# Kernel optimization log

Hardware: AMD Instinct MI355X
Metric: run time of the kernel (lower is better)

## Reference

```python
import jax, jax.numpy as jnp
import numpy as np

DIM = 256
HEADS = 4
HEAD_DIM = DIM // HEADS
WIN_DIC = {512: 16, 256: 16, 128: 8, 64: 8, 32: 4, 16: 4}


def window_partition(x, w):
    # x: [B, C, H, W] -> [B*nH*nW, w*w, C]
    B, C, H, W = x.shape
    x = x.reshape(B, C, H // w, w, W // w, w)
    x = jnp.transpose(x, (0, 2, 4, 3, 5, 1))
    return x.reshape(-1, w * w, C)


def window_reverse(windows, w, H, W, C):
    # windows: [B*nH*nW, w*w, C] -> [B, C, H, W]
    B = windows.shape[0] // ((H // w) * (W // w))
    x = windows.reshape(B, H // w, W // w, w, w, C)
    x = jnp.transpose(x, (0, 5, 1, 3, 2, 4))
    return x.reshape(B, C, H, W)


def setup_inputs() -> dict:
    key = jax.random.key(0)
    ks = jax.random.split(key, 10)
    B, C, H, W = 8, DIM, 128, 128
    feat_a = jax.random.normal(ks[0], (B, C, H, W), dtype=jnp.float32)
    feat_b = jax.random.normal(ks[1], (B, C, H, W), dtype=jnp.float32)
    s = 1.0 / np.sqrt(DIM)
    Wq = jax.random.normal(ks[2], (DIM, DIM), dtype=jnp.float32) * s
    bq = jnp.zeros((DIM,), dtype=jnp.float32)
    Wk = jax.random.normal(ks[3], (DIM, DIM), dtype=jnp.float32) * s
    bk = jnp.zeros((DIM,), dtype=jnp.float32)
    Wv = jax.random.normal(ks[4], (DIM, DIM), dtype=jnp.float32) * s
    bv = jnp.zeros((DIM,), dtype=jnp.float32)
    Wo = jax.random.normal(ks[5], (DIM, DIM), dtype=jnp.float32) * s
    bo = jnp.zeros((DIM,), dtype=jnp.float32)
    return {"feat_a": feat_a, "feat_b": feat_b, "Wq": Wq, "bq": bq,
            "Wk": Wk, "bk": bk, "Wv": Wv, "bv": bv, "Wo": Wo, "bo": bo}


def reference(feat_a, feat_b, Wq, bq, Wk, bk, Wv, bv, Wo, bo):
    B, C, H, W = feat_a.shape
    w = WIN_DIC[H]
    pad_h = (w - H % w) % w
    pad_w = (w - W % w) % w
    if pad_h or pad_w:
        feat_a = jnp.pad(feat_a, ((0, 0), (0, 0), (0, pad_h), (0, pad_w)), mode="reflect")
        feat_b = jnp.pad(feat_b, ((0, 0), (0, 0), (0, pad_h), (0, pad_w)), mode="reflect")
    Hp, Wp = feat_a.shape[2], feat_a.shape[3]

    qw = window_partition(feat_a, w)   # [B_, N, C]
    kw = window_partition(feat_b, w)
    # Linear (torch nn.Linear: x @ W.T + b)
    q = qw @ Wq.T + bq
    k = kw @ Wk.T + bk
    v = kw @ Wv.T + bv

    B_, N, _ = q.shape
    q = q.reshape(B_, N, HEADS, HEAD_DIM).transpose(0, 2, 1, 3)  # [B_, h, N, d]
    k = k.reshape(B_, N, HEADS, HEAD_DIM).transpose(0, 2, 1, 3)
    v = v.reshape(B_, N, HEADS, HEAD_DIM).transpose(0, 2, 1, 3)

    scale = HEAD_DIM ** -0.5
    attn = jnp.einsum("bhnd,bhmd->bhnm", q, k) * scale
    attn = jax.nn.softmax(attn, axis=-1)  # dropout is identity in eval mode
    out = jnp.einsum("bhnm,bhmd->bhnd", attn, v)
    out = out.transpose(0, 2, 1, 3).reshape(B_, N, C)
    out = out @ Wo.T + bo
    out = window_reverse(out, w, Hp, Wp, C)
    out = out[:, :, :H, :W]
    return (out, attn)
```

## Files before the change

### kernel.cpp

```cpp
#include <hip/hip_runtime.h>
#include <hip/hip_bf16.h>


typedef __bf16 bf16x8 __attribute__((ext_vector_type(8)));
typedef float f32x4 __attribute__((ext_vector_type(4)));
typedef unsigned short u16;
typedef unsigned short u16x8 __attribute__((ext_vector_type(8)));

#define MFMA16(A, B, C) __builtin_amdgcn_mfma_f32_16x16x32_bf16((A), (B), (C), 0, 0, 0)

__device__ __forceinline__ int swzA(int t, int byteInRow) {
    return (t << 9) + (byteInRow ^ ((((t & 7) ^ (t >> 3)) & 7) << 4));
}
__device__ __forceinline__ int swzB(int r, int byteInRow) {
    return (r << 7) + (byteInRow ^ ((((r & 7) ^ (r >> 3)) & 7) << 4));
}

__global__ __launch_bounds__(256) void pack_weights(
    const float* __restrict__ Wq, const float* __restrict__ Wk,
    const float* __restrict__ Wv, const float* __restrict__ Wo,
    __bf16* __restrict__ pk)
{
    int gid = blockIdx.x * 256 + threadIdx.x;
    int m = gid >> 13;
    int f = gid & 8191;
    const float* W = (m == 0) ? Wq : (m == 1) ? Wk : (m == 2) ? Wv : Wo;
    int q  = f >> 11;
    int kk = (f >> 8) & 7;
    int t16 = (f >> 6) & 3;
    int l  = f & 63;
    int row = (q << 6) + (t16 << 4) + (l & 15);
    int col = (kk << 5) + ((l >> 4) << 3);
    const float* s = W + row * 256 + col;
    f32x4 a = *(const f32x4*)s;
    f32x4 b = *(const f32x4*)(s + 4);
    bf16x8 r;
    r[0] = (__bf16)a[0]; r[1] = (__bf16)a[1]; r[2] = (__bf16)a[2]; r[3] = (__bf16)a[3];
    r[4] = (__bf16)b[0]; r[5] = (__bf16)b[1]; r[6] = (__bf16)b[2]; r[7] = (__bf16)b[3];
    *(bf16x8*)(pk + (size_t)gid * 8) = r;
}

__device__ __forceinline__ bf16x8 loadWP(const __bf16* __restrict__ pk,
                                         int q, int kk, int t16, int l) {
    return *(const bf16x8*)(pk + ((((q << 3) + kk) << 2) + t16) * 512 + (l << 3));
}

__global__ __launch_bounds__(512) void wca_fused(
    const float* __restrict__ fa, const float* __restrict__ fb,
    const __bf16* __restrict__ WPq, const float* __restrict__ bq,
    const __bf16* __restrict__ WPk, const float* __restrict__ bk,
    const __bf16* __restrict__ WPv, const float* __restrict__ bv,
    const __bf16* __restrict__ WPo, const float* __restrict__ bo,
    float* __restrict__ outg, float* __restrict__ attng)
{
    __shared__ __attribute__((aligned(16))) char S[131072];
    char* const XA = S;
    char* const XB = S + 32768;
    char* const QQ = S + 65536;
    char* const KK = S + 98304;

    const int tid  = threadIdx.x;
    const int l    = tid & 63;
    const int wid  = tid >> 6;
    const int lrow = l & 15;
    const int kg   = l >> 4;
    const int q    = wid & 3;
    const int th   = wid >> 2;

    const int wgid = blockIdx.x;
    const int win  = ((wgid & 7) << 8) | (wgid >> 3);
    const int b    = win >> 8;
    const int wy   = (win >> 4) & 15;
    const int wx   = win & 15;
    const int ybase = wy << 3, xbase = wx << 3;

    {
        #pragma unroll
        for (int f = 0; f < 2; ++f) {
            const float* src = f ? fb : fa;
            char* dst = f ? XB : XA;
            #pragma unroll
            for (int it = 0; it < 4; ++it) {
                int idx = (it << 9) + tid;
                int c  = idx >> 3;
                int ty = idx & 7;
                const float* gp = src + ((((size_t)b * 256 + c) * 128 + ybase + ty) * 128 + xbase);
                f32x4 v0 = *(const f32x4*)gp;
                f32x4 v1 = *(const f32x4*)(gp + 4);
                #pragma unroll
                for (int tx = 0; tx < 4; ++tx) {
                    int t0 = (ty << 3) + tx;
                    int t1 = (ty << 3) + 4 + tx;
                    *(__bf16*)(dst + swzA(t0, c << 1)) = (__bf16)v0[tx];
                    *(__bf16*)(dst + swzA(t1, c << 1)) = (__bf16)v1[tx];
                }
            }
        }
    }
    __syncthreads();

    {
        #pragma unroll
        for (int pp = 0; pp < 2; ++pp) {
            const __bf16* WP  = pp ? WPk : WPq;
            const float* bias = pp ? bk : bq;
            const char* Xs  = pp ? XB : XA;
            char* dstR      = pp ? KK : QQ;
            f32x4 acc[2][4] = {};
            #pragma unroll
            for (int kk = 0; kk < 8; ++kk) {
                int c0 = (kk << 5) + (kg << 3);
                bf16x8 a0 = *(const bf16x8*)(Xs + swzA((th << 5) + lrow,      c0 << 1));
                bf16x8 a1 = *(const bf16x8*)(Xs + swzA((th << 5) + 16 + lrow, c0 << 1));
                #pragma unroll
                for (int nt = 0; nt < 4; ++nt) {
                    bf16x8 bb = loadWP(WP, q, kk, nt, l);
                    acc[0][nt] = MFMA16(a0, bb, acc[0][nt]);
                    acc[1][nt] = MFMA16(a1, bb, acc[1][nt]);
                }
            }
            #pragma unroll
            for (int mt = 0; mt < 2; ++mt) {
                #pragma unroll
                for (int nt = 0; nt < 4; ++nt) {
                    int co = (q << 6) + (nt << 4) + lrow;
                    float bi = bias[co];
                    #pragma unroll
                    for (int r = 0; r < 4; ++r) {
                        int t = (th << 5) + (mt << 4) + (kg << 2) + r;
                        *(__bf16*)(dstR + swzA(t, co << 1)) = (__bf16)(acc[mt][nt][r] + bi);
                    }
                }
            }
        }
    }
    __syncthreads();

    {
        const int h = q;
        f32x4 s[2][4] = {};
        #pragma unroll
        for (int kk = 0; kk < 2; ++kk) {
            int c0 = (h << 6) + (kk << 5) + (kg << 3);
            bf16x8 a0 = *(const bf16x8*)(QQ + swzA((th << 5) + lrow,      c0 << 1));
            bf16x8 a1 = *(const bf16x8*)(QQ + swzA((th << 5) + 16 + lrow, c0 << 1));
            #pragma unroll
            for (int nt = 0; nt < 4; ++nt) {
                bf16x8 kb = *(const bf16x8*)(KK + swzA((nt << 4) + lrow, c0 << 1));
                s[0][nt] = MFMA16(a0, kb, s[0][nt]);
                s[1][nt] = MFMA16(a1, kb, s[1][nt]);
            }
        }
        const float CS = 0.125f * 1.44269504f;
        #pragma unroll
        for (int mt = 0; mt < 2; ++mt) {
            #pragma unroll
            for (int r = 0; r < 4; ++r) {
                float mx = fmaxf(fmaxf(s[mt][0][r], s[mt][1][r]),
                                 fmaxf(s[mt][2][r], s[mt][3][r]));
                mx = fmaxf(mx, __shfl_xor(mx, 1));
                mx = fmaxf(mx, __shfl_xor(mx, 2));
                mx = fmaxf(mx, __shfl_xor(mx, 4));
                mx = fmaxf(mx, __shfl_xor(mx, 8));
                float p0 = exp2f((s[mt][0][r] - mx) * CS);
                float p1 = exp2f((s[mt][1][r] - mx) * CS);
                float p2 = exp2f((s[mt][2][r] - mx) * CS);
                float p3 = exp2f((s[mt][3][r] - mx) * CS);
                float sm = (p0 + p1) + (p2 + p3);
                sm += __shfl_xor(sm, 1);
                sm += __shfl_xor(sm, 2);
                sm += __shfl_xor(sm, 4);
                sm += __shfl_xor(sm, 8);
                float inv = 1.0f / sm;
                int i = (th << 5) + (mt << 4) + (kg << 2) + r;
                char* pb = XA + (h << 13);
                *(__bf16*)(pb + swzB(i, ((0 << 4) + lrow) << 1)) = (__bf16)(p0 * inv);
                *(__bf16*)(pb + swzB(i, ((1 << 4) + lrow) << 1)) = (__bf16)(p1 * inv);
                *(__bf16*)(pb + swzB(i, ((2 << 4) + lrow) << 1)) = (__bf16)(p2 * inv);
                *(__bf16*)(pb + swzB(i, ((3 << 4) + lrow) << 1)) = (__bf16)(p3 * inv);
            }
        }
    }
    __syncthreads();

    {
        f32x4 acc[4][2] = {};
        #pragma unroll
        for (int kk = 0; kk < 8; ++kk) {
            int c0 = (kk << 5) + (kg << 3);
            bf16x8 bx0 = *(const bf16x8*)(XB + swzA((th << 5) + lrow,      c0 << 1));
            bf16x8 bx1 = *(const bf16x8*)(XB + swzA((th << 5) + 16 + lrow, c0 << 1));
            #pragma unroll
            for (int mt = 0; mt < 4; ++mt) {
                bf16x8 aw = loadWP(WPv, q, kk, mt, l);
                acc[mt][0] = MFMA16(aw, bx0, acc[mt][0]);
                acc[mt][1] = MFMA16(aw, bx1, acc[mt][1]);
            }
        }
        #pragma unroll
        for (int mt = 0; mt < 4; ++mt) {
            #pragma unroll
            for (int r = 0; r < 4; ++r) {
                int vc = (q << 6) + (mt << 4) + (kg << 2) + r;
                float bi = bv[vc];
                #pragma unroll
                for (int nt = 0; nt < 2; ++nt) {
                    int t = (th << 5) + (nt << 4) + lrow;
                    *(__bf16*)(QQ + swzB(vc, t << 1)) = (__bf16)(acc[mt][nt][r] + bi);
                }
            }
        }
        #pragma unroll
        for (int it = 0; it < 4; ++it) {
            int idx = (it << 9) + tid;
            int h2 = idx >> 9;
            int i2 = (idx >> 3) & 63;
            int jb = (idx & 7) << 3;
            u16x8 v = *(const u16x8*)(XA + (h2 << 13) + swzB(i2, jb << 1));
            float* dp = attng + ((((size_t)(win << 2) + h2) << 6) + i2) * 64 + jb;
            f32x4 o0, o1;
            #pragma unroll
            for (int e = 0; e < 4; ++e) {
                union { unsigned u; float f; } c0; c0.u = (unsigned)v[e] << 16;
                union { unsigned u; float f; } c1; c1.u = (unsigned)v[4 + e] << 16;
                o0[e] = c0.f; o1[e] = c1.f;
            }
            *(f32x4*)dp = o0;
            *(f32x4*)(dp + 4) = o1;
        }
    }
    __syncthreads();

    {
        const int h = q;
        f32x4 o[2][4] = {};
        #pragma unroll
        for (int kk = 0; kk < 2; ++kk) {
            int j0 = (kk << 5) + (kg << 3);
            bf16x8 a0 = *(const bf16x8*)(XA + (h << 13) + swzB((th << 5) + lrow,      j0 << 1));
            bf16x8 a1 = *(const bf16x8*)(XA + (h << 13) + swzB((th << 5) + 16 + lrow, j0 << 1));
            #pragma unroll
            for (int dt = 0; dt < 4; ++dt) {
                bf16x8 vb = *(const bf16x8*)(QQ + swzB((h << 6) + (dt << 4) + lrow, j0 << 1));
                o[0][dt] = MFMA16(a0, vb, o[0][dt]);
                o[1][dt] = MFMA16(a1, vb, o[1][dt]);
            }
        }
        #pragma unroll
        for (int mt = 0; mt < 2; ++mt) {
            #pragma unroll
            for (int dt = 0; dt < 4; ++dt) {
                #pragma unroll
                for (int r = 0; r < 4; ++r) {
                    int t = (th << 5) + (mt << 4) + (kg << 2) + r;
                    int c = (h << 6) + (dt << 4) + lrow;
                    *(__bf16*)(KK + swzA(t, c << 1)) = (__bf16)o[mt][dt][r];
                }
            }
        }
    }
    __syncthreads();

    {
        f32x4 acc[4][2] = {};
        #pragma unroll
        for (int kk = 0; kk < 8; ++kk) {
            int k0 = (kk << 5) + (kg << 3);
            bf16x8 b0 = *(const bf16x8*)(KK + swzA((th << 5) + lrow,      k0 << 1));
            bf16x8 b1 = *(const bf16x8*)(KK + swzA((th << 5) + 16 + lrow, k0 << 1));
            #pragma unroll
            for (int mt = 0; mt < 4; ++mt) {
                bf16x8 aw = loadWP(WPo, q, kk, mt, l);
                acc[mt][0] = MFMA16(aw, b0, acc[mt][0]);
                acc[mt][1] = MFMA16(aw, b1, acc[mt][1]);
            }
        }
        #pragma unroll
        for (int mt = 0; mt < 4; ++mt) {
            #pragma unroll
            for (int r = 0; r < 4; ++r) {
                int c = (q << 6) + (mt << 4) + (kg << 2) + r;
                float bi = bo[c];
                #pragma unroll
                for (int nt = 0; nt < 2; ++nt) {
                    int t = (th << 5) + (nt << 4) + lrow;
                    int y = ybase + (t >> 3);
                    int x = xbase + (t & 7);
                    size_t off = (((size_t)b * 256 + c) * 128 + y) * 128 + x;
                    outg[off] = acc[mt][nt][r] + bi;
                }
            }
        }
    }
}

extern "C" void kernel_launch(void* const* d_in, const int* in_sizes, int n_in,
                              void* d_out, int out_size, void* d_ws, size_t ws_size,
                              hipStream_t stream) {
    (void)in_sizes; (void)n_in; (void)ws_size; (void)out_size;
    const float* fa = (const float*)d_in[0];
    const float* fb = (const float*)d_in[1];
    const float* Wq = (const float*)d_in[2];
    const float* bq = (const float*)d_in[3];
    const float* Wk = (const float*)d_in[4];
    const float* bk = (const float*)d_in[5];
    const float* Wv = (const float*)d_in[6];
    const float* bv = (const float*)d_in[7];
    const float* Wo = (const float*)d_in[8];
    const float* bo = (const float*)d_in[9];
    float* outg  = (float*)d_out;
    float* attng = outg + (size_t)8 * 256 * 128 * 128;

    __bf16* pk = (__bf16*)d_ws;
    const __bf16* WPq = pk;
    const __bf16* WPk = pk + 65536;
    const __bf16* WPv = pk + 131072;
    const __bf16* WPo = pk + 196608;

    pack_weights<<<dim3(128), dim3(256), 0, stream>>>(Wq, Wk, Wv, Wo, pk);
    wca_fused<<<dim3(2048), dim3(512), 0, stream>>>(
        fa, fb, WPq, bq, WPk, bk, WPv, bv, WPo, bo, outg, attng);
}
```

Measured before the change: 310.4 us.

## Halve LDS footprint by holding K, V, P in registers and reusing two regions

Shared memory per block shrinks from 128 KB to 64 KB. The K, V and softmax P results are held in packed bf16 registers across barriers, and two LDS regions are reused for each stage, so more workgroups can be resident per CU. The launch bounds now request 4 waves per SIMD. Attention probabilities are written to global as fp32 directly from registers instead of through an LDS round trip, and the values are no longer rounded to bf16. The cost is more barriers, higher register pressure and less coalesced scattered global stores for attn.

```diff
diff --git a/kernel.cpp b/kernel.cpp
--- a/kernel.cpp
+++ b/kernel.cpp
@@ -5,7 +5,6 @@
 typedef __bf16 bf16x8 __attribute__((ext_vector_type(8)));
 typedef float f32x4 __attribute__((ext_vector_type(4)));
 typedef unsigned short u16;
-typedef unsigned short u16x8 __attribute__((ext_vector_type(8)));
 
 #define MFMA16(A, B, C) __builtin_amdgcn_mfma_f32_16x16x32_bf16((A), (B), (C), 0, 0, 0)
 
@@ -14,6 +13,10 @@
 }
 __device__ __forceinline__ int swzB(int r, int byteInRow) {
     return (r << 7) + (byteInRow ^ ((((r & 7) ^ (r >> 3)) & 7) << 4));
+}
+__device__ __forceinline__ u16 bfbits(float x) {
+    __bf16 h = (__bf16)x;
+    return *(u16*)&h;
 }
 
 __global__ __launch_bounds__(256) void pack_weights(
@@ -45,7 +48,7 @@
     return *(const bf16x8*)(pk + ((((q << 3) + kk) << 2) + t16) * 512 + (l << 3));
 }
 
-__global__ __launch_bounds__(512) void wca_fused(
+__global__ __launch_bounds__(512, 4) void wca_fused(
     const float* __restrict__ fa, const float* __restrict__ fb,
     const __bf16* __restrict__ WPq, const float* __restrict__ bq,
     const __bf16* __restrict__ WPk, const float* __restrict__ bk,
@@ -53,11 +56,9 @@
     const __bf16* __restrict__ WPo, const float* __restrict__ bo,
     float* __restrict__ outg, float* __restrict__ attng)
 {
-    __shared__ __attribute__((aligned(16))) char S[131072];
-    char* const XA = S;
-    char* const XB = S + 32768;
-    char* const QQ = S + 65536;
-    char* const KK = S + 98304;
+    __shared__ __attribute__((aligned(16))) char S[65536];
+    char* const R1 = S;
+    char* const R2 = S + 32768;
 
     const int tid  = threadIdx.x;
     const int l    = tid & 63;
@@ -78,7 +79,7 @@
         #pragma unroll
         for (int f = 0; f < 2; ++f) {
             const float* src = f ? fb : fa;
-            char* dst = f ? XB : XA;
+            char* dst = f ? R2 : R1;
             #pragma unroll
             for (int it = 0; it < 4; ++it) {
                 int idx = (it << 9) + tid;
@@ -89,64 +90,133 @@
                 f32x4 v1 = *(const f32x4*)(gp + 4);
                 #pragma unroll
                 for (int tx = 0; tx < 4; ++tx) {
-                    int t0 = (ty << 3) + tx;
-                    int t1 = (ty << 3) + 4 + tx;
-                    *(__bf16*)(dst + swzA(t0, c << 1)) = (__bf16)v0[tx];
-                    *(__bf16*)(dst + swzA(t1, c << 1)) = (__bf16)v1[tx];
-                }
-            }
-        }
-    }
-    __syncthreads();
-
-    {
-        #pragma unroll
-        for (int pp = 0; pp < 2; ++pp) {
-            const __bf16* WP  = pp ? WPk : WPq;
-            const float* bias = pp ? bk : bq;
-            const char* Xs  = pp ? XB : XA;
-            char* dstR      = pp ? KK : QQ;
-            f32x4 acc[2][4] = {};
+                    *(__bf16*)(dst + swzA((ty << 3) + tx,     c << 1)) = (__bf16)v0[tx];
+                    *(__bf16*)(dst + swzA((ty << 3) + 4 + tx, c << 1)) = (__bf16)v1[tx];
+                }
+            }
+        }
+    }
+    __syncthreads();
+
+    f32x4 qacc[2][4] = {};
+    {
+        #pragma unroll
+        for (int kk = 0; kk < 8; ++kk) {
+            int c0 = (kk << 5) + (kg << 3);
+            bf16x8 a0 = *(const bf16x8*)(R1 + swzA((th << 5) + lrow,      c0 << 1));
+            bf16x8 a1 = *(const bf16x8*)(R1 + swzA((th << 5) + 16 + lrow, c0 << 1));
+            #pragma unroll
+            for (int nt = 0; nt < 4; ++nt) {
+                bf16x8 bb = loadWP(WPq, q, kk, nt, l);
+                qacc[0][nt] = MFMA16(a0, bb, qacc[0][nt]);
+                qacc[1][nt] = MFMA16(a1, bb, qacc[1][nt]);
+            }
+        }
+    }
+    __syncthreads();
+
+    unsigned kpk[16], vpk[16];
+    {
+        #pragma unroll
+        for (int mt = 0; mt < 2; ++mt) {
+            #pragma unroll
+            for (int nt = 0; nt < 4; ++nt) {
+                int co = (q << 6) + (nt << 4) + lrow;
+                float bi = bq[co];
+                #pragma unroll
+                for (int r = 0; r < 4; ++r) {
+                    int t = (th << 5) + (mt << 4) + (kg << 2) + r;
+                    *(__bf16*)(R1 + swzA(t, co << 1)) = (__bf16)(qacc[mt][nt][r] + bi);
+                }
+            }
+        }
+        {
+            f32x4 kacc[2][4] = {};
             #pragma unroll
             for (int kk = 0; kk < 8; ++kk) {
                 int c0 = (kk << 5) + (kg << 3);
-                bf16x8 a0 = *(const bf16x8*)(Xs + swzA((th << 5) + lrow,      c0 << 1));
-                bf16x8 a1 = *(const bf16x8*)(Xs + swzA((th << 5) + 16 + lrow, c0 << 1));
+                bf16x8 a0 = *(const bf16x8*)(R2 + swzA((th << 5) + lrow,      c0 << 1));
+                bf16x8 a1 = *(const bf16x8*)(R2 + swzA((th << 5) + 16 + lrow, c0 << 1));
                 #pragma unroll
                 for (int nt = 0; nt < 4; ++nt) {
-                    bf16x8 bb = loadWP(WP, q, kk, nt, l);
-                    acc[0][nt] = MFMA16(a0, bb, acc[0][nt]);
-                    acc[1][nt] = MFMA16(a1, bb, acc[1][nt]);
+                    bf16x8 bb = loadWP(WPk, q, kk, nt, l);
+                    kacc[0][nt] = MFMA16(a0, bb, kacc[0][nt]);
+                    kacc[1][nt] = MFMA16(a1, bb, kacc[1][nt]);
                 }
             }
             #pragma unroll
             for (int mt = 0; mt < 2; ++mt) {
                 #pragma unroll
                 for (int nt = 0; nt < 4; ++nt) {
-                    int co = (q << 6) + (nt << 4) + lrow;
-                    float bi = bias[co];
-                    #pragma unroll
-                    for (int r = 0; r < 4; ++r) {
-                        int t = (th << 5) + (mt << 4) + (kg << 2) + r;
-                        *(__bf16*)(dstR + swzA(t, co << 1)) = (__bf16)(acc[mt][nt][r] + bi);
-                    }
-                }
-            }
-        }
-    }
-    __syncthreads();
-
+                    float bi = bk[(q << 6) + (nt << 4) + lrow];
+                    kpk[(mt * 4 + nt) * 2 + 0] =
+                        (unsigned)bfbits(kacc[mt][nt][0] + bi) |
+                        ((unsigned)bfbits(kacc[mt][nt][1] + bi) << 16);
+                    kpk[(mt * 4 + nt) * 2 + 1] =
+                        (unsigned)bfbits(kacc[mt][nt][2] + bi) |
+                        ((unsigned)bfbits(kacc[mt][nt][3] + bi) << 16);
+                }
+            }
+        }
+        {
+            f32x4 vacc[4][2] = {};
+            #pragma unroll
+            for (int kk = 0; kk < 8; ++kk) {
+                int c0 = (kk << 5) + (kg << 3);
+                bf16x8 bx0 = *(const bf16x8*)(R2 + swzA((th << 5) + lrow,      c0 << 1));
+                bf16x8 bx1 = *(const bf16x8*)(R2 + swzA((th << 5) + 16 + lrow, c0 << 1));
+                #pragma unroll
+                for (int mt = 0; mt < 4; ++mt) {
+                    bf16x8 aw = loadWP(WPv, q, kk, mt, l);
+                    vacc[mt][0] = MFMA16(aw, bx0, vacc[mt][0]);
+                    vacc[mt][1] = MFMA16(aw, bx1, vacc[mt][1]);
+                }
+            }
+            #pragma unroll
+            for (int mt = 0; mt < 4; ++mt) {
+                #pragma unroll
+                for (int nt = 0; nt < 2; ++nt) {
+                    u16 w0 = bfbits(vacc[mt][nt][0] + bv[(q << 6) + (mt << 4) + (kg << 2) + 0]);
+                    u16 w1 = bfbits(vacc[mt][nt][1] + bv[(q << 6) + (mt << 4) + (kg << 2) + 1]);
+                    u16 w2 = bfbits(vacc[mt][nt][2] + bv[(q << 6) + (mt << 4) + (kg << 2) + 2]);
+                    u16 w3 = bfbits(vacc[mt][nt][3] + bv[(q << 6) + (mt << 4) + (kg << 2) + 3]);
+                    vpk[(mt * 2 + nt) * 2 + 0] = (unsigned)w0 | ((unsigned)w1 << 16);
+                    vpk[(mt * 2 + nt) * 2 + 1] = (unsigned)w2 | ((unsigned)w3 << 16);
+                }
+            }
+        }
+    }
+    __syncthreads();
+
+    {
+        #pragma unroll
+        for (int mt = 0; mt < 2; ++mt) {
+            #pragma unroll
+            for (int nt = 0; nt < 4; ++nt) {
+                int co = (q << 6) + (nt << 4) + lrow;
+                #pragma unroll
+                for (int r = 0; r < 4; ++r) {
+                    int t = (th << 5) + (mt << 4) + (kg << 2) + r;
+                    u16 val = (u16)(kpk[(mt * 4 + nt) * 2 + (r >> 1)] >> ((r & 1) * 16));
+                    *(u16*)(R2 + swzA(t, co << 1)) = val;
+                }
+            }
+        }
+    }
+    __syncthreads();
+
+    unsigned ppk[16];
     {
         const int h = q;
         f32x4 s[2][4] = {};
         #pragma unroll
         for (int kk = 0; kk < 2; ++kk) {
             int c0 = (h << 6) + (kk << 5) + (kg << 3);
-            bf16x8 a0 = *(const bf16x8*)(QQ + swzA((th << 5) + lrow,      c0 << 1));
-            bf16x8 a1 = *(const bf16x8*)(QQ + swzA((th << 5) + 16 + lrow, c0 << 1));
+            bf16x8 a0 = *(const bf16x8*)(R1 + swzA((th << 5) + lrow,      c0 << 1));
+            bf16x8 a1 = *(const bf16x8*)(R1 + swzA((th << 5) + 16 + lrow, c0 << 1));
             #pragma unroll
             for (int nt = 0; nt < 4; ++nt) {
-                bf16x8 kb = *(const bf16x8*)(KK + swzA((nt << 4) + lrow, c0 << 1));
+                bf16x8 kb = *(const bf16x8*)(R2 + swzA((nt << 4) + lrow, c0 << 1));
                 s[0][nt] = MFMA16(a0, kb, s[0][nt]);
                 s[1][nt] = MFMA16(a1, kb, s[1][nt]);
             }
@@ -172,29 +242,29 @@
                 sm += __shfl_xor(sm, 4);
                 sm += __shfl_xor(sm, 8);
                 float inv = 1.0f / sm;
+                p0 *= inv; p1 *= inv; p2 *= inv; p3 *= inv;
                 int i = (th << 5) + (mt << 4) + (kg << 2) + r;
-                char* pb = XA + (h << 13);
-                *(__bf16*)(pb + swzB(i, ((0 << 4) + lrow) << 1)) = (__bf16)(p0 * inv);
-                *(__bf16*)(pb + swzB(i, ((1 << 4) + lrow) << 1)) = (__bf16)(p1 * inv);
-                *(__bf16*)(pb + swzB(i, ((2 << 4) + lrow) << 1)) = (__bf16)(p2 * inv);
-                *(__bf16*)(pb + swzB(i, ((3 << 4) + lrow) << 1)) = (__bf16)(p3 * inv);
-            }
-        }
-    }
-    __syncthreads();
-
-    {
-        f32x4 acc[4][2] = {};
-        #pragma unroll
-        for (int kk = 0; kk < 8; ++kk) {
-            int c0 = (kk << 5) + (kg << 3);
-            bf16x8 bx0 = *(const bf16x8*)(XB + swzA((th << 5) + lrow,      c0 << 1));
-            bf16x8 bx1 = *(const bf16x8*)(XB + swzA((th << 5) + 16 + lrow, c0 << 1));
-            #pragma unroll
-            for (int mt = 0; mt < 4; ++mt) {
-                bf16x8 aw = loadWP(WPv, q, kk, mt, l);
-                acc[mt][0] = MFMA16(aw, bx0, acc[mt][0]);
-                acc[mt][1] = MFMA16(aw, bx1, acc[mt][1]);
+                float* ap = attng + (((size_t)(win << 2) + h) * 64 + i) * 64 + lrow;
+                ap[0] = p0; ap[16] = p1; ap[32] = p2; ap[48] = p3;
+                ppk[(mt * 4 + r) * 2 + 0] = (unsigned)bfbits(p0) | ((unsigned)bfbits(p1) << 16);
+                ppk[(mt * 4 + r) * 2 + 1] = (unsigned)bfbits(p2) | ((unsigned)bfbits(p3) << 16);
+            }
+        }
+    }
+    __syncthreads();
+
+    {
+        const int h = q;
+        #pragma unroll
+        for (int mt = 0; mt < 2; ++mt) {
+            #pragma unroll
+            for (int r = 0; r < 4; ++r) {
+                int i = (th << 5) + (mt << 4) + (kg << 2) + r;
+                #pragma unroll
+                for (int nt = 0; nt < 4; ++nt) {
+                    u16 val = (u16)(ppk[(mt * 4 + r) * 2 + (nt >> 1)] >> ((nt & 1) * 16));
+                    *(u16*)(R2 + (h << 13) + swzB(i, ((nt << 4) + lrow) << 1)) = val;
+                }
             }
         }
         #pragma unroll
@@ -202,50 +272,37 @@
             #pragma unroll
             for (int r = 0; r < 4; ++r) {
                 int vc = (q << 6) + (mt << 4) + (kg << 2) + r;
-                float bi = bv[vc];
                 #pragma unroll
                 for (int nt = 0; nt < 2; ++nt) {
                     int t = (th << 5) + (nt << 4) + lrow;
-                    *(__bf16*)(QQ + swzB(vc, t << 1)) = (__bf16)(acc[mt][nt][r] + bi);
-                }
-            }
-        }
-        #pragma unroll
-        for (int it = 0; it < 4; ++it) {
-            int idx = (it << 9) + tid;
-            int h2 = idx >> 9;
-            int i2 = (idx >> 3) & 63;
-            int jb = (idx & 7) << 3;
-            u16x8 v = *(const u16x8*)(XA + (h2 << 13) + swzB(i2, jb << 1));
-            float* dp = attng + ((((size_t)(win << 2) + h2) << 6) + i2) * 64 + jb;
-            f32x4 o0, o1;
-            #pragma unroll
-            for (int e = 0; e < 4; ++e) {
-                union { unsigned u; float f; } c0; c0.u = (unsigned)v[e] << 16;
-                union { unsigned u; float f; } c1; c1.u = (unsigned)v[4 + e] << 16;
-                o0[e] = c0.f; o1[e] = c1.f;
-            }
-            *(f32x4*)dp = o0;
-            *(f32x4*)(dp + 4) = o1;
-        }
-    }
-    __syncthreads();
-
+                    u16 val = (u16)(vpk[(mt * 2 + nt) * 2 + (r >> 1)] >> ((r & 1) * 16));
+                    *(u16*)(R1 + swzB(vc, t << 1)) = val;
+                }
+            }
+        }
+    }
+    __syncthreads();
+
+    f32x4 o[2][4] = {};
     {
         const int h = q;
-        f32x4 o[2][4] = {};
         #pragma unroll
         for (int kk = 0; kk < 2; ++kk) {
             int j0 = (kk << 5) + (kg << 3);
-            bf16x8 a0 = *(const bf16x8*)(XA + (h << 13) + swzB((th << 5) + lrow,      j0 << 1));
-            bf16x8 a1 = *(const bf16x8*)(XA + (h << 13) + swzB((th << 5) + 16 + lrow, j0 << 1));
+            bf16x8 a0 = *(const bf16x8*)(R2 + (h << 13) + swzB((th << 5) + lrow,      j0 << 1));
+            bf16x8 a1 = *(const bf16x8*)(R2 + (h << 13) + swzB((th << 5) + 16 + lrow, j0 << 1));
             #pragma unroll
             for (int dt = 0; dt < 4; ++dt) {
-                bf16x8 vb = *(const bf16x8*)(QQ + swzB((h << 6) + (dt << 4) + lrow, j0 << 1));
+                bf16x8 vb = *(const bf16x8*)(R1 + swzB((h << 6) + (dt << 4) + lrow, j0 << 1));
                 o[0][dt] = MFMA16(a0, vb, o[0][dt]);
                 o[1][dt] = MFMA16(a1, vb, o[1][dt]);
             }
         }
+    }
+    __syncthreads();
+
+    {
+        const int h = q;
         #pragma unroll
         for (int mt = 0; mt < 2; ++mt) {
             #pragma unroll
@@ -254,7 +311,7 @@
                 for (int r = 0; r < 4; ++r) {
                     int t = (th << 5) + (mt << 4) + (kg << 2) + r;
                     int c = (h << 6) + (dt << 4) + lrow;
-                    *(__bf16*)(KK + swzA(t, c << 1)) = (__bf16)o[mt][dt][r];
+                    *(__bf16*)(R1 + swzA(t, c << 1)) = (__bf16)o[mt][dt][r];
                 }
             }
         }
@@ -266,8 +323,8 @@
         #pragma unroll
         for (int kk = 0; kk < 8; ++kk) {
             int k0 = (kk << 5) + (kg << 3);
-            bf16x8 b0 = *(const bf16x8*)(KK + swzA((th << 5) + lrow,      k0 << 1));
-            bf16x8 b1 = *(const bf16x8*)(KK + swzA((th << 5) + 16 + lrow, k0 << 1));
+            bf16x8 b0 = *(const bf16x8*)(R1 + swzA((th << 5) + lrow,      k0 << 1));
+            bf16x8 b1 = *(const bf16x8*)(R1 + swzA((th << 5) + 16 + lrow, k0 << 1));
             #pragma unroll
             for (int mt = 0; mt < 4; ++mt) {
                 bf16x8 aw = loadWP(WPo, q, kk, mt, l);
```

After: 485.5 us. 56.4% more time.

## Reorder stages and shared buffers, request two workgroups per CU

Applied to the files above, without the earlier changes.

Adds a launch bound of two 512-thread workgroups per CU and reschedules the fused kernel. The V projection now runs right after Q/K, the attention probabilities go into the freed feat_b buffer, and the P·V product is merged into the same phase as the attention write-out, removing one barrier. The goal is fewer synchronisations and more resident waves. The 128 KB static shared allocation per workgroup may still prevent two workgroups from fitting on a CU, and the tighter register cap could cause spills.

```diff
diff --git a/kernel.cpp b/kernel.cpp
--- a/kernel.cpp
+++ b/kernel.cpp
@@ -45,7 +45,7 @@
     return *(const bf16x8*)(pk + ((((q << 3) + kk) << 2) + t16) * 512 + (l << 3));
 }
 
-__global__ __launch_bounds__(512) void wca_fused(
+__global__ __launch_bounds__(512, 2) void wca_fused(
     const float* __restrict__ fa, const float* __restrict__ fb,
     const __bf16* __restrict__ WPq, const float* __restrict__ bq,
     const __bf16* __restrict__ WPk, const float* __restrict__ bk,
@@ -54,10 +54,10 @@
     float* __restrict__ outg, float* __restrict__ attng)
 {
     __shared__ __attribute__((aligned(16))) char S[131072];
-    char* const XA = S;
-    char* const XB = S + 32768;
-    char* const QQ = S + 65536;
-    char* const KK = S + 98304;
+    char* const A = S;
+    char* const B = S + 32768;
+    char* const C = S + 65536;
+    char* const D = S + 98304;
 
     const int tid  = threadIdx.x;
     const int l    = tid & 63;
@@ -78,7 +78,7 @@
         #pragma unroll
         for (int f = 0; f < 2; ++f) {
             const float* src = f ? fb : fa;
-            char* dst = f ? XB : XA;
+            char* dst = f ? B : A;
             #pragma unroll
             for (int it = 0; it < 4; ++it) {
                 int idx = (it << 9) + tid;
@@ -89,47 +89,94 @@
                 f32x4 v1 = *(const f32x4*)(gp + 4);
                 #pragma unroll
                 for (int tx = 0; tx < 4; ++tx) {
-                    int t0 = (ty << 3) + tx;
-                    int t1 = (ty << 3) + 4 + tx;
-                    *(__bf16*)(dst + swzA(t0, c << 1)) = (__bf16)v0[tx];
-                    *(__bf16*)(dst + swzA(t1, c << 1)) = (__bf16)v1[tx];
-                }
-            }
-        }
-    }
-    __syncthreads();
-
-    {
-        #pragma unroll
-        for (int pp = 0; pp < 2; ++pp) {
-            const __bf16* WP  = pp ? WPk : WPq;
-            const float* bias = pp ? bk : bq;
-            const char* Xs  = pp ? XB : XA;
-            char* dstR      = pp ? KK : QQ;
-            f32x4 acc[2][4] = {};
-            #pragma unroll
-            for (int kk = 0; kk < 8; ++kk) {
-                int c0 = (kk << 5) + (kg << 3);
-                bf16x8 a0 = *(const bf16x8*)(Xs + swzA((th << 5) + lrow,      c0 << 1));
-                bf16x8 a1 = *(const bf16x8*)(Xs + swzA((th << 5) + 16 + lrow, c0 << 1));
-                #pragma unroll
-                for (int nt = 0; nt < 4; ++nt) {
-                    bf16x8 bb = loadWP(WP, q, kk, nt, l);
-                    acc[0][nt] = MFMA16(a0, bb, acc[0][nt]);
-                    acc[1][nt] = MFMA16(a1, bb, acc[1][nt]);
-                }
-            }
-            #pragma unroll
-            for (int mt = 0; mt < 2; ++mt) {
-                #pragma unroll
-                for (int nt = 0; nt < 4; ++nt) {
-                    int co = (q << 6) + (nt << 4) + lrow;
-                    float bi = bias[co];
-                    #pragma unroll
-                    for (int r = 0; r < 4; ++r) {
-                        int t = (th << 5) + (mt << 4) + (kg << 2) + r;
-                        *(__bf16*)(dstR + swzA(t, co << 1)) = (__bf16)(acc[mt][nt][r] + bi);
-                    }
+                    *(__bf16*)(dst + swzA((ty << 3) + tx,     c << 1)) = (__bf16)v0[tx];
+                    *(__bf16*)(dst + swzA((ty << 3) + 4 + tx, c << 1)) = (__bf16)v1[tx];
+                }
+            }
+        }
+    }
+    __syncthreads();
+
+    {
+        f32x4 qacc[2][4] = {};
+        #pragma unroll
+        for (int kk = 0; kk < 8; ++kk) {
+            int c0 = (kk << 5) + (kg << 3);
+            bf16x8 a0 = *(const bf16x8*)(A + swzA((th << 5) + lrow,      c0 << 1));
+            bf16x8 a1 = *(const bf16x8*)(A + swzA((th << 5) + 16 + lrow, c0 << 1));
+            #pragma unroll
+            for (int nt = 0; nt < 4; ++nt) {
+                bf16x8 bb = loadWP(WPq, q, kk, nt, l);
+                qacc[0][nt] = MFMA16(a0, bb, qacc[0][nt]);
+                qacc[1][nt] = MFMA16(a1, bb, qacc[1][nt]);
+            }
+        }
+        #pragma unroll
+        for (int mt = 0; mt < 2; ++mt) {
+            #pragma unroll
+            for (int nt = 0; nt < 4; ++nt) {
+                int co = (q << 6) + (nt << 4) + lrow;
+                float bi = bq[co];
+                #pragma unroll
+                for (int r = 0; r < 4; ++r) {
+                    int t = (th << 5) + (mt << 4) + (kg << 2) + r;
+                    *(__bf16*)(C + swzA(t, co << 1)) = (__bf16)(qacc[mt][nt][r] + bi);
+                }
+            }
+        }
+        f32x4 kacc[2][4] = {};
+        #pragma unroll
+        for (int kk = 0; kk < 8; ++kk) {
+            int c0 = (kk << 5) + (kg << 3);
+            bf16x8 a0 = *(const bf16x8*)(B + swzA((th << 5) + lrow,      c0 << 1));
+            bf16x8 a1 = *(const bf16x8*)(B + swzA((th << 5) + 16 + lrow, c0 << 1));
+            #pragma unroll
+            for (int nt = 0; nt < 4; ++nt) {
+                bf16x8 bb = loadWP(WPk, q, kk, nt, l);
+                kacc[0][nt] = MFMA16(a0, bb, kacc[0][nt]);
+                kacc[1][nt] = MFMA16(a1, bb, kacc[1][nt]);
+            }
+        }
+        #pragma unroll
+        for (int mt = 0; mt < 2; ++mt) {
+            #pragma unroll
+            for (int nt = 0; nt < 4; ++nt) {
+                int co = (q << 6) + (nt << 4) + lrow;
+                float bi = bk[co];
+                #pragma unroll
+                for (int r = 0; r < 4; ++r) {
+                    int t = (th << 5) + (mt << 4) + (kg << 2) + r;
+                    *(__bf16*)(D + swzA(t, co << 1)) = (__bf16)(kacc[mt][nt][r] + bi);
+                }
+            }
+        }
+    }
+    __syncthreads();
+
+    {
+        f32x4 vacc[4][2] = {};
+        #pragma unroll
+        for (int kk = 0; kk < 8; ++kk) {
+            int c0 = (kk << 5) + (kg << 3);
+            bf16x8 bx0 = *(const bf16x8*)(B + swzA((th << 5) + lrow,      c0 << 1));
+            bf16x8 bx1 = *(const bf16x8*)(B + swzA((th << 5) + 16 + lrow, c0 << 1));
+            #pragma unroll
+            for (int mt = 0; mt < 4; ++mt) {
+                bf16x8 aw = loadWP(WPv, q, kk, mt, l);
+                vacc[mt][0] = MFMA16(aw, bx0, vacc[mt][0]);
+                vacc[mt][1] = MFMA16(aw, bx1, vacc[mt][1]);
+            }
+        }
+        #pragma unroll
+        for (int mt = 0; mt < 4; ++mt) {
+            #pragma unroll
+            for (int r = 0; r < 4; ++r) {
+                int vc = (q << 6) + (mt << 4) + (kg << 2) + r;
+                float bi = bv[vc];
+                #pragma unroll
+                for (int nt = 0; nt < 2; ++nt) {
+                    int t = (th << 5) + (nt << 4) + lrow;
+                    *(__bf16*)(A + swzB(vc, t << 1)) = (__bf16)(vacc[mt][nt][r] + bi);
                 }
             }
         }
@@ -142,16 +189,17 @@
         #pragma unroll
         for (int kk = 0; kk < 2; ++kk) {
             int c0 = (h << 6) + (kk << 5) + (kg << 3);
-            bf16x8 a0 = *(const bf16x8*)(QQ + swzA((th << 5) + lrow,      c0 << 1));
-            bf16x8 a1 = *(const bf16x8*)(QQ + swzA((th << 5) + 16 + lrow, c0 << 1));
-            #pragma unroll
-            for (int nt = 0; nt < 4; ++nt) {
-                bf16x8 kb = *(const bf16x8*)(KK + swzA((nt << 4) + lrow, c0 << 1));
+            bf16x8 a0 = *(const bf16x8*)(C + swzA((th << 5) + lrow,      c0 << 1));
+            bf16x8 a1 = *(const bf16x8*)(C + swzA((th << 5) + 16 + lrow, c0 << 1));
+            #pragma unroll
+            for (int nt = 0; nt < 4; ++nt) {
+                bf16x8 kb = *(const bf16x8*)(D + swzA((nt << 4) + lrow, c0 << 1));
                 s[0][nt] = MFMA16(a0, kb, s[0][nt]);
                 s[1][nt] = MFMA16(a1, kb, s[1][nt]);
             }
         }
         const float CS = 0.125f * 1.44269504f;
+        char* pb = B + (h << 13);
         #pragma unroll
         for (int mt = 0; mt < 2; ++mt) {
             #pragma unroll
@@ -173,7 +221,6 @@
                 sm += __shfl_xor(sm, 8);
                 float inv = 1.0f / sm;
                 int i = (th << 5) + (mt << 4) + (kg << 2) + r;
-                char* pb = XA + (h << 13);
                 *(__bf16*)(pb + swzB(i, ((0 << 4) + lrow) << 1)) = (__bf16)(p0 * inv);
                 *(__bf16*)(pb + swzB(i, ((1 << 4) + lrow) << 1)) = (__bf16)(p1 * inv);
                 *(__bf16*)(pb + swzB(i, ((2 << 4) + lrow) << 1)) = (__bf16)(p2 * inv);
@@ -184,29 +231,29 @@
     __syncthreads();
 
     {
-        f32x4 acc[4][2] = {};
-        #pragma unroll
-        for (int kk = 0; kk < 8; ++kk) {
-            int c0 = (kk << 5) + (kg << 3);
-            bf16x8 bx0 = *(const bf16x8*)(XB + swzA((th << 5) + lrow,      c0 << 1));
-            bf16x8 bx1 = *(const bf16x8*)(XB + swzA((th << 5) + 16 + lrow, c0 << 1));
-            #pragma unroll
-            for (int mt = 0; mt < 4; ++mt) {
-                bf16x8 aw = loadWP(WPv, q, kk, mt, l);
-                acc[mt][0] = MFMA16(aw, bx0, acc[mt][0]);
-                acc[mt][1] = MFMA16(aw, bx1, acc[mt][1]);
-            }
-        }
-        #pragma unroll
-        for (int mt = 0; mt < 4; ++mt) {
-            #pragma unroll
-            for (int r = 0; r < 4; ++r) {
-                int vc = (q << 6) + (mt << 4) + (kg << 2) + r;
-                float bi = bv[vc];
-                #pragma unroll
-                for (int nt = 0; nt < 2; ++nt) {
-                    int t = (th << 5) + (nt << 4) + lrow;
-                    *(__bf16*)(QQ + swzB(vc, t << 1)) = (__bf16)(acc[mt][nt][r] + bi);
+        const int h = q;
+        f32x4 o[2][4] = {};
+        #pragma unroll
+        for (int kk = 0; kk < 2; ++kk) {
+            int j0 = (kk << 5) + (kg << 3);
+            bf16x8 a0 = *(const bf16x8*)(B + (h << 13) + swzB((th << 5) + lrow,      j0 << 1));
+            bf16x8 a1 = *(const bf16x8*)(B + (h << 13) + swzB((th << 5) + 16 + lrow, j0 << 1));
+            #pragma unroll
+            for (int dt = 0; dt < 4; ++dt) {
+                bf16x8 vb = *(const bf16x8*)(A + swzB((h << 6) + (dt << 4) + lrow, j0 << 1));
+                o[0][dt] = MFMA16(a0, vb, o[0][dt]);
+                o[1][dt] = MFMA16(a1, vb, o[1][dt]);
+            }
+        }
+        #pragma unroll
+        for (int mt = 0; mt < 2; ++mt) {
+            #pragma unroll
+            for (int dt = 0; dt < 4; ++dt) {
+                #pragma unroll
+                for (int r = 0; r < 4; ++r) {
+                    int t = (th << 5) + (mt << 4) + (kg << 2) + r;
+                    int c = (h << 6) + (dt << 4) + lrow;
+                    *(__bf16*)(C + swzA(t, c << 1)) = (__bf16)o[mt][dt][r];
                 }
             }
         }
@@ -216,7 +263,7 @@
             int h2 = idx >> 9;
             int i2 = (idx >> 3) & 63;
             int jb = (idx & 7) << 3;
-            u16x8 v = *(const u16x8*)(XA + (h2 << 13) + swzB(i2, jb << 1));
+            u16x8 v = *(const u16x8*)(B + (h2 << 13) + swzB(i2, jb << 1));
             float* dp = attng + ((((size_t)(win << 2) + h2) << 6) + i2) * 64 + jb;
             f32x4 o0, o1;
             #pragma unroll
@@ -232,42 +279,12 @@
     __syncthreads();
 
     {
-        const int h = q;
-        f32x4 o[2][4] = {};
-        #pragma unroll
-        for (int kk = 0; kk < 2; ++kk) {
-            int j0 = (kk << 5) + (kg << 3);
-            bf16x8 a0 = *(const bf16x8*)(XA + (h << 13) + swzB((th << 5) + lrow,      j0 << 1));
-            bf16x8 a1 = *(const bf16x8*)(XA + (h << 13) + swzB((th << 5) + 16 + lrow, j0 << 1));
-            #pragma unroll
-            for (int dt = 0; dt < 4; ++dt) {
-                bf16x8 vb = *(const bf16x8*)(QQ + swzB((h << 6) + (dt << 4) + lrow, j0 << 1));
-                o[0][dt] = MFMA16(a0, vb, o[0][dt]);
-                o[1][dt] = MFMA16(a1, vb, o[1][dt]);
-            }
-        }
-        #pragma unroll
-        for (int mt = 0; mt < 2; ++mt) {
-            #pragma unroll
-            for (int dt = 0; dt < 4; ++dt) {
-                #pragma unroll
-                for (int r = 0; r < 4; ++r) {
-                    int t = (th << 5) + (mt << 4) + (kg << 2) + r;
-                    int c = (h << 6) + (dt << 4) + lrow;
-                    *(__bf16*)(KK + swzA(t, c << 1)) = (__bf16)o[mt][dt][r];
-                }
-            }
-        }
-    }
-    __syncthreads();
-
-    {
         f32x4 acc[4][2] = {};
         #pragma unroll
         for (int kk = 0; kk < 8; ++kk) {
             int k0 = (kk << 5) + (kg << 3);
-            bf16x8 b0 = *(const bf16x8*)(KK + swzA((th << 5) + lrow,      k0 << 1));
-            bf16x8 b1 = *(const bf16x8*)(KK + swzA((th << 5) + 16 + lrow, k0 << 1));
+            bf16x8 b0 = *(const bf16x8*)(C + swzA((th << 5) + lrow,      k0 << 1));
+            bf16x8 b1 = *(const bf16x8*)(C + swzA((th << 5) + 16 + lrow, k0 << 1));
             #pragma unroll
             for (int mt = 0; mt < 4; ++mt) {
                 bf16x8 aw = loadWP(WPo, q, kk, mt, l);
```

After: 311.1 us. Within noise of the previous version (+0.2%).
